# Optimization experiments

Measured on AMD Instinct MI355X. Metric: run time of the kernel, lower is better.

Reference implementation:

```python
import jax, jax.numpy as jnp
import numpy as np

B, N, HID, E, H = 4, 256, 256, 64, 4
OUT = HID // 2          # 128
D = OUT // H            # 32
AGG = H * (2 * D + 1)   # 260 = concat(mean D, attn_sum 1, max D) per head


def setup_inputs() -> dict:
    key = jax.random.key(0)
    ks = jax.random.split(key, 7)
    s = 0.05
    return {
        "h_x": jax.random.normal(ks[0], (B, N, HID), jnp.float32),
        "h_e": jax.random.normal(ks[1], (B, N, N, E), jnp.float32),
        "h_m": jnp.ones((B, N), jnp.float32),
        "W_Q": jax.random.normal(ks[2], (OUT, HID), jnp.float32) * s,
        "W_K": jax.random.normal(ks[3], (OUT, E), jnp.float32) * s,
        "W_V": jax.random.normal(ks[4], (OUT, E), jnp.float32) * s,
        "W_R": jax.random.normal(ks[5], (OUT, AGG), jnp.float32) * s,
    }


def reference(h_x, h_e, h_m, W_Q, W_K, W_V, W_R):
    # queries from node features: [B,H,N,D]
    h_q = (h_x @ W_Q.T).reshape(B, N, H, D).transpose(0, 2, 1, 3)
    # keys/values from dense pairwise edge features: [B,H,N,N,D]
    h_k = jnp.einsum('bnme,ce->bnmc', h_e, W_K).reshape(B, N, N, H, D).transpose(0, 3, 1, 2, 4)
    h_v = jnp.einsum('bnme,ce->bnmc', h_e, W_V).reshape(B, N, N, H, D).transpose(0, 3, 1, 2, 4)
    # broadcast dot: [B,H,N,N]
    scores = jnp.einsum('bhnd,bhnmd->bhnm', h_q, h_k) / np.float32(np.sqrt(D))
    # per-node mask broadcast as [B,1,N,1] (masks query rows)
    scores = jnp.where(h_m[:, None, :, None] == 0, -jnp.inf, scores)
    # NOTE: original code softmaxes over dim=1 = HEAD axis (faithful)
    attn = jax.nn.softmax(scores, axis=1)                      # [B,H,N,N]
    attn_w = attn[..., None] * h_v                             # [B,H,N,N,D]
    aggr_sum = attn_w.sum(axis=3)                              # [B,H,N,D]
    attn_sum = attn.sum(axis=3, keepdims=True) + 1e-8          # [B,H,N,1]
    aggr_mean = aggr_sum / attn_sum
    aggr_max = attn_w.max(axis=3)                              # [B,H,N,D]
    multi = jnp.concatenate([aggr_mean, attn_sum, aggr_max], axis=-1)  # [B,H,N,2D+1]
    aggr_out = multi.transpose(0, 2, 1, 3).reshape(B, N, AGG)  # [B,N,260]
    return aggr_out @ W_R.T                                    # [B,N,OUT]
```

## Files before the change

### kernel.cpp

```cpp
#include <hip/hip_runtime.h>
#include <hip/hip_bf16.h>

constexpr int Bb   = 4;
constexpr int Nn   = 256;
constexpr int HID  = 256;
constexpr int Ee   = 64;
constexpr int Hh   = 4;
constexpr int OUTc = 128;
constexpr int Dd   = 32;
constexpr int AGG  = 260;
constexpr int REC  = 264;
constexpr int QA_LD = 264;

constexpr size_t WS_WRT   = 0;
constexpr size_t WS_FRAGV = WS_WRT + (size_t)AGG * OUTc;
constexpr size_t WS_FRAGQ = WS_FRAGV + 4096;
constexpr size_t WS_UFRAG = WS_FRAGQ + 16384;

typedef __attribute__((ext_vector_type(8))) short short8;
typedef __attribute__((ext_vector_type(4))) float floatx4;

__device__ __forceinline__ unsigned pk2(float a, float b) {
    union { __hip_bfloat162 h; unsigned u; } cv;
    cv.h = __float22bfloat162_rn(float2{a, b});
    return cv.u;
}

__device__ __forceinline__ short8 pack8(floatx4 f0, floatx4 f1) {
    union { short8 s; unsigned u[4]; } r;
    r.u[0] = pk2(f0[0], f0[1]);
    r.u[1] = pk2(f0[2], f0[3]);
    r.u[2] = pk2(f1[0], f1[1]);
    r.u[3] = pk2(f1[2], f1[3]);
    return r.s;
}

__device__ __forceinline__ void gload16(const float* g, float* l) {
    __builtin_amdgcn_global_load_lds(
        (const __attribute__((address_space(1))) void*)g,
        (__attribute__((address_space(3))) void*)l, 16, 0, 0);
}

__global__ __launch_bounds__(256)
void eama_prep(const float* __restrict__ W_Q, const float* __restrict__ W_V,
               const float* __restrict__ W_R, const float* __restrict__ h_x,
               const float* __restrict__ W_K,
               unsigned short* __restrict__ wfragV, float* __restrict__ W_RT,
               unsigned short* __restrict__ ufrag)
{
    __shared__ __align__(16) unsigned short sA[16 * QA_LD];
    __shared__ __align__(16) float sqL[16][132];
    __shared__ __align__(16) float sU2[16][256];

    const int tid = threadIdx.x;
    const int bid = blockIdx.x;

    if (bid < 4) {
        const int e    = bid * 256 + tid;
        const int lane = e & 63;
        const int ks   = (e >> 6) & 1;
        const int ct   = e >> 7;
        const int ncol = lane & 15, q8 = lane >> 4;
        const float* row = W_V + (ct * 16 + ncol) * Ee;
        const int k0 = ks * 32 + q8 * 8;
        floatx4 f0 = *(const floatx4*)(row + k0);
        floatx4 f1 = *(const floatx4*)(row + k0 + 4);
        *(short8*)(wfragV + (size_t)e * 8) = pack8(f0, f1);
        return;
    }
    if (bid < 134) {
        const int i = (bid - 4) * 256 + tid;
        if (i < AGG * OUTc) {
            const int c = i & 127, j = i >> 7;
            W_RT[j * OUTc + c] = W_R[c * AGG + j];
        }
        return;
    }

    const int b0   = (bid - 134) * 16;
    const int lane = tid & 63;
    const int wv   = tid >> 6;
    const int ncol = lane & 15, q8 = lane >> 4;

    short8 bq[2][8];
    #pragma unroll
    for (int ct = 0; ct < 2; ++ct)
        #pragma unroll
        for (int ks = 0; ks < 8; ++ks) {
            const float* row = W_Q + (size_t)(wv * 32 + ct * 16 + ncol) * HID + ks * 32 + q8 * 8;
            bq[ct][ks] = pack8(*(const floatx4*)row, *(const floatx4*)(row + 4));
        }
    #pragma unroll
    for (int i = 0; i < 2; ++i) {
        const int idx = tid + i * 256;
        const int r = idx >> 5, blk = idx & 31;
        const float* src = h_x + (size_t)(b0 + r) * HID + blk * 8;
        floatx4 f0 = *(const floatx4*)(src);
        floatx4 f1 = *(const floatx4*)(src + 4);
        *(short8*)&sA[r * QA_LD + blk * 8] = pack8(f0, f1);
    }
    __syncthreads();
    floatx4 acc[2] = {(floatx4){0,0,0,0}, (floatx4){0,0,0,0}};
    #pragma unroll
    for (int ks = 0; ks < 8; ++ks) {
        short8 a = *(const short8*)&sA[ncol * QA_LD + ks * 32 + q8 * 8];
        acc[0] = __builtin_amdgcn_mfma_f32_16x16x32_bf16(a, bq[0][ks], acc[0], 0, 0, 0);
        acc[1] = __builtin_amdgcn_mfma_f32_16x16x32_bf16(a, bq[1][ks], acc[1], 0, 0, 0);
    }
    #pragma unroll
    for (int ct = 0; ct < 2; ++ct)
        #pragma unroll
        for (int rr = 0; rr < 4; ++rr)
            sqL[q8 * 4 + rr][wv * 32 + ct * 16 + ncol] = acc[ct][rr];
    __syncthreads();

    {
        const int h = wv, e = lane;
        float a16[16];
        #pragma unroll
        for (int i = 0; i < 16; ++i) a16[i] = 0.f;
        #pragma unroll
        for (int d4 = 0; d4 < 8; ++d4) {
            float wk0 = W_K[(h * Dd + d4 * 4 + 0) * Ee + e];
            float wk1 = W_K[(h * Dd + d4 * 4 + 1) * Ee + e];
            float wk2 = W_K[(h * Dd + d4 * 4 + 2) * Ee + e];
            float wk3 = W_K[(h * Dd + d4 * 4 + 3) * Ee + e];
            #pragma unroll
            for (int b16 = 0; b16 < 16; ++b16) {
                floatx4 qv = *(const floatx4*)&sqL[b16][h * Dd + d4 * 4];
                a16[b16] += (qv[0] * wk0 + qv[1] * wk1) + (qv[2] * wk2 + qv[3] * wk3);
            }
        }
        #pragma unroll
        for (int b16 = 0; b16 < 16; ++b16)
            sU2[b16][h * 64 + e] = a16[b16] * 0.1767766952966369f;
    }
    __syncthreads();

    #pragma unroll
    for (int k = 0; k < 8; ++k) {
        const int ei   = tid + k * 256;
        const int b16  = ei >> 7;
        const int rest = ei & 127;
        const int ks   = rest >> 6;
        const int l    = rest & 63;
        const int nc   = l & 15, qq = l >> 4;
        short8 v = {0, 0, 0, 0, 0, 0, 0, 0};
        if (nc < Hh) {
            floatx4 f0 = *(const floatx4*)&sU2[b16][nc * 64 + ks * 32 + qq * 8];
            floatx4 f1 = *(const floatx4*)&sU2[b16][nc * 64 + ks * 32 + qq * 8 + 4];
            v = pack8(f0, f1);
        }
        *(short8*)(ufrag + ((size_t)((b0 + b16) * 2 + ks) * 64 + l) * 8) = v;
    }
}

__global__ __launch_bounds__(256, 2)
void eama_full(const float* __restrict__ h_e, const float* __restrict__ h_m,
               const unsigned short* __restrict__ wfragV,
               const unsigned short* __restrict__ ufrag,
               const float* __restrict__ W_RT, float* __restrict__ out)
{
    __shared__ __align__(16) float sStage[4][2][4][64][4];
    __shared__ __align__(16) float sS[4][16][4];
    __shared__ float sVS[4][OUTc];
    __shared__ float sVM[4][OUTc];
    __shared__ float sAS[4][Hh];
    __shared__ float sAsum[Hh];

    float* sM = &sStage[0][0][0][0][0];
    float (*sAcc)[OUTc] = (float (*)[OUTc])(sM + 384);

    const int tid  = threadIdx.x;
    const int lane = tid & 63;
    const int w    = tid >> 6;
    const int ncol = lane & 15;
    const int q8   = lane >> 4;
    const int bn   = blockIdx.x;
    const float maskv = h_m[bn];

    short8 bfV[8][2];
    #pragma unroll
    for (int ct = 0; ct < 8; ++ct)
        #pragma unroll
        for (int ks = 0; ks < 2; ++ks)
            bfV[ct][ks] = *(const short8*)(wfragV + ((size_t)(ct * 2 + ks) * 64 + lane) * 8);
    short8 bu0 = *(const short8*)(ufrag + ((size_t)(bn * 2 + 0) * 64 + lane) * 8);
    short8 bu1 = *(const short8*)(ufrag + ((size_t)(bn * 2 + 1) * 64 + lane) * 8);
    asm volatile("" ::: "memory");

    const float* heb = h_e + (size_t)bn * Nn * Ee;
    const float* arq = heb + (size_t)(w * 64 + ncol) * Ee + q8 * 8;

    #define STAGE(it_, buf_) do { \
        const float* ar_ = arq + (size_t)(it_) * 16 * Ee; \
        gload16(ar_,      &sStage[w][buf_][0][0][0]); \
        gload16(ar_ + 4,  &sStage[w][buf_][1][0][0]); \
        gload16(ar_ + 32, &sStage[w][buf_][2][0][0]); \
        gload16(ar_ + 36, &sStage[w][buf_][3][0][0]); \
    } while (0)

    STAGE(0, 0);
    STAGE(1, 1);

    float vs[8], vm[8], asumH = 0.f;
    #pragma unroll
    for (int ct = 0; ct < 8; ++ct) { vs[ct] = 0.f; vm[ct] = -3.402823466e38f; }

    #pragma unroll
    for (int it = 0; it < 4; ++it) {
        const int buf = it & 1;
        if (it < 3) asm volatile("s_waitcnt vmcnt(4)" ::: "memory");
        else        asm volatile("s_waitcnt vmcnt(0)" ::: "memory");

        floatx4 c0 = *(const floatx4*)&sStage[w][buf][0][lane][0];
        floatx4 c1 = *(const floatx4*)&sStage[w][buf][1][lane][0];
        floatx4 c2 = *(const floatx4*)&sStage[w][buf][2][lane][0];
        floatx4 c3 = *(const floatx4*)&sStage[w][buf][3][lane][0];
        short8 af0 = pack8(c0, c1);
        short8 af1 = pack8(c2, c3);
        if (it < 2) {
            asm volatile("s_waitcnt lgkmcnt(0)" ::: "memory");
            STAGE(it + 2, buf);
        }

        floatx4 accV[8], accS = (floatx4){0, 0, 0, 0};
        #pragma unroll
        for (int ct = 0; ct < 8; ++ct) accV[ct] = (floatx4){0, 0, 0, 0};
        #pragma unroll
        for (int ct = 0; ct < 8; ++ct) {
            accV[ct] = __builtin_amdgcn_mfma_f32_16x16x32_bf16(af0, bfV[ct][0], accV[ct], 0, 0, 0);
            accV[ct] = __builtin_amdgcn_mfma_f32_16x16x32_bf16(af1, bfV[ct][1], accV[ct], 0, 0, 0);
        }
        accS = __builtin_amdgcn_mfma_f32_16x16x32_bf16(af0, bu0, accS, 0, 0, 0);
        accS = __builtin_amdgcn_mfma_f32_16x16x32_bf16(af1, bu1, accS, 0, 0, 0);

        if (ncol < Hh) {
            #pragma unroll
            for (int r = 0; r < 4; ++r)
                sS[w][q8 * 4 + r][ncol] = (maskv != 0.f) ? accS[r] : -1e30f;
        }
        __builtin_amdgcn_wave_barrier();

        #pragma unroll
        for (int r = 0; r < 4; ++r) {
            floatx4 sc = *(const floatx4*)&sS[w][q8 * 4 + r][0];
            float e0 = __expf(sc[0]), e1 = __expf(sc[1]);
            float e2 = __expf(sc[2]), e3 = __expf(sc[3]);
            float inv = 1.f / ((e0 + e1) + (e2 + e3));
            float a0 = e0 * inv, a1 = e1 * inv, a2 = e2 * inv, a3 = e3 * inv;
            asumH += (ncol & 2) ? ((ncol & 1) ? a3 : a2) : ((ncol & 1) ? a1 : a0);
            float p;
            p = a0 * accV[0][r]; vs[0] += p; vm[0] = fmaxf(vm[0], p);
            p = a0 * accV[1][r]; vs[1] += p; vm[1] = fmaxf(vm[1], p);
            p = a1 * accV[2][r]; vs[2] += p; vm[2] = fmaxf(vm[2], p);
            p = a1 * accV[3][r]; vs[3] += p; vm[3] = fmaxf(vm[3], p);
            p = a2 * accV[4][r]; vs[4] += p; vm[4] = fmaxf(vm[4], p);
            p = a2 * accV[5][r]; vs[5] += p; vm[5] = fmaxf(vm[5], p);
            p = a3 * accV[6][r]; vs[6] += p; vm[6] = fmaxf(vm[6], p);
            p = a3 * accV[7][r]; vs[7] += p; vm[7] = fmaxf(vm[7], p);
        }
        __builtin_amdgcn_wave_barrier();
    }
    #undef STAGE

    #pragma unroll
    for (int ct = 0; ct < 8; ++ct) {
        vs[ct] += __shfl_xor(vs[ct], 16, 64);
        vs[ct] += __shfl_xor(vs[ct], 32, 64);
        vm[ct] = fmaxf(vm[ct], __shfl_xor(vm[ct], 16, 64));
        vm[ct] = fmaxf(vm[ct], __shfl_xor(vm[ct], 32, 64));
    }
    asumH += __shfl_xor(asumH, 16, 64);
    asumH += __shfl_xor(asumH, 32, 64);

    if (lane < 16) {
        #pragma unroll
        for (int ct = 0; ct < 8; ++ct) {
            sVS[w][ct * 16 + lane] = vs[ct];
            sVM[w][ct * 16 + lane] = vm[ct];
        }
    }
    if (lane < Hh) sAS[w][lane] = asumH;
    __syncthreads();
    if (tid < Hh) {
        sAsum[tid] = 1e-8f +
            (sAS[0][tid] + sAS[1][tid]) + (sAS[2][tid] + sAS[3][tid]);
    }
    __syncthreads();
    if (tid < OUTc) {
        float vsum = (sVS[0][tid] + sVS[1][tid]) + (sVS[2][tid] + sVS[3][tid]);
        float vmax = fmaxf(fmaxf(sVM[0][tid], sVM[1][tid]), fmaxf(sVM[2][tid], sVM[3][tid]));
        const int h = tid >> 5, d = tid & 31;
        sM[h * 65 + d]      = vsum / sAsum[h];
        sM[h * 65 + 33 + d] = vmax;
        if (tid < Hh) sM[tid * 65 + 32] = sAsum[tid];
    }
    __syncthreads();
    {
        const int c = tid & 127, part = tid >> 7;
        const int j0 = part * 130;
        float a0 = 0.f, a1 = 0.f, a2 = 0.f, a3 = 0.f;
        #pragma unroll 4
        for (int j = j0; j < j0 + 128; j += 4) {
            a0 = fmaf(sM[j],     W_RT[(j)     * OUTc + c], a0);
            a1 = fmaf(sM[j + 1], W_RT[(j + 1) * OUTc + c], a1);
            a2 = fmaf(sM[j + 2], W_RT[(j + 2) * OUTc + c], a2);
            a3 = fmaf(sM[j + 3], W_RT[(j + 3) * OUTc + c], a3);
        }
        a0 = fmaf(sM[j0 + 128], W_RT[(j0 + 128) * OUTc + c], a0);
        a1 = fmaf(sM[j0 + 129], W_RT[(j0 + 129) * OUTc + c], a1);
        sAcc[part][c] = (a0 + a1) + (a2 + a3);
    }
    __syncthreads();
    if (tid < OUTc)
        out[bn * OUTc + tid] = sAcc[0][tid] + sAcc[1][tid];
}

extern "C" void kernel_launch(void* const* d_in, const int* in_sizes, int n_in,
                              void* d_out, int out_size, void* d_ws, size_t ws_size,
                              hipStream_t stream) {
    const float* h_x = (const float*)d_in[0];
    const float* h_e = (const float*)d_in[1];
    const float* h_m = (const float*)d_in[2];
    const float* W_Q = (const float*)d_in[3];
    const float* W_K = (const float*)d_in[4];
    const float* W_V = (const float*)d_in[5];
    const float* W_R = (const float*)d_in[6];
    float* out = (float*)d_out;

    float* ws            = (float*)d_ws;
    float* W_RT          = ws + WS_WRT;
    unsigned short* wfV  = (unsigned short*)(ws + WS_FRAGV);
    unsigned short* ufr  = (unsigned short*)(ws + WS_UFRAG);

    eama_prep<<<dim3(198), dim3(256), 0, stream>>>(W_Q, W_V, W_R, h_x, W_K, wfV, W_RT, ufr);
    eama_full<<<dim3(Bb * Nn), dim3(256), 0, stream>>>(h_e, h_m, wfV, ufr, W_RT, out);
}
```

Measured before the change: 127.4 us.

## Fuse prep kernel into main kernel, computing Q/U and V fragments per block

Removes the separate prep launch. Each block now builds its own W_V bf16 fragments through shared memory, computes its query row with W_Q and folds it with W_K into the score vector U. The output projection reads W_R directly with strided vector loads instead of a pre-transposed copy. This drops one launch, the workspace round trip and the dependency between the two kernels. In exchange every block redoes the weight packing and the small GEMVs, which adds redundant global loads and extra barriers before the main loop. Those prologue loads are issued after the first h_e stages, so they can overlap with them.

```diff
diff --git a/kernel.cpp b/kernel.cpp
--- a/kernel.cpp
+++ b/kernel.cpp
@@ -9,16 +9,10 @@
 constexpr int OUTc = 128;
 constexpr int Dd   = 32;
 constexpr int AGG  = 260;
-constexpr int REC  = 264;
-constexpr int QA_LD = 264;
-
-constexpr size_t WS_WRT   = 0;
-constexpr size_t WS_FRAGV = WS_WRT + (size_t)AGG * OUTc;
-constexpr size_t WS_FRAGQ = WS_FRAGV + 4096;
-constexpr size_t WS_UFRAG = WS_FRAGQ + 16384;
 
 typedef __attribute__((ext_vector_type(8))) short short8;
 typedef __attribute__((ext_vector_type(4))) float floatx4;
+typedef __attribute__((ext_vector_type(2))) float floatx2;
 
 __device__ __forceinline__ unsigned pk2(float a, float b) {
     union { __hip_bfloat162 h; unsigned u; } cv;
@@ -41,135 +35,17 @@
         (__attribute__((address_space(3))) void*)l, 16, 0, 0);
 }
 
-__global__ __launch_bounds__(256)
-void eama_prep(const float* __restrict__ W_Q, const float* __restrict__ W_V,
-               const float* __restrict__ W_R, const float* __restrict__ h_x,
-               const float* __restrict__ W_K,
-               unsigned short* __restrict__ wfragV, float* __restrict__ W_RT,
-               unsigned short* __restrict__ ufrag)
-{
-    __shared__ __align__(16) unsigned short sA[16 * QA_LD];
-    __shared__ __align__(16) float sqL[16][132];
-    __shared__ __align__(16) float sU2[16][256];
-
-    const int tid = threadIdx.x;
-    const int bid = blockIdx.x;
-
-    if (bid < 4) {
-        const int e    = bid * 256 + tid;
-        const int lane = e & 63;
-        const int ks   = (e >> 6) & 1;
-        const int ct   = e >> 7;
-        const int ncol = lane & 15, q8 = lane >> 4;
-        const float* row = W_V + (ct * 16 + ncol) * Ee;
-        const int k0 = ks * 32 + q8 * 8;
-        floatx4 f0 = *(const floatx4*)(row + k0);
-        floatx4 f1 = *(const floatx4*)(row + k0 + 4);
-        *(short8*)(wfragV + (size_t)e * 8) = pack8(f0, f1);
-        return;
-    }
-    if (bid < 134) {
-        const int i = (bid - 4) * 256 + tid;
-        if (i < AGG * OUTc) {
-            const int c = i & 127, j = i >> 7;
-            W_RT[j * OUTc + c] = W_R[c * AGG + j];
-        }
-        return;
-    }
-
-    const int b0   = (bid - 134) * 16;
-    const int lane = tid & 63;
-    const int wv   = tid >> 6;
-    const int ncol = lane & 15, q8 = lane >> 4;
-
-    short8 bq[2][8];
-    #pragma unroll
-    for (int ct = 0; ct < 2; ++ct)
-        #pragma unroll
-        for (int ks = 0; ks < 8; ++ks) {
-            const float* row = W_Q + (size_t)(wv * 32 + ct * 16 + ncol) * HID + ks * 32 + q8 * 8;
-            bq[ct][ks] = pack8(*(const floatx4*)row, *(const floatx4*)(row + 4));
-        }
-    #pragma unroll
-    for (int i = 0; i < 2; ++i) {
-        const int idx = tid + i * 256;
-        const int r = idx >> 5, blk = idx & 31;
-        const float* src = h_x + (size_t)(b0 + r) * HID + blk * 8;
-        floatx4 f0 = *(const floatx4*)(src);
-        floatx4 f1 = *(const floatx4*)(src + 4);
-        *(short8*)&sA[r * QA_LD + blk * 8] = pack8(f0, f1);
-    }
-    __syncthreads();
-    floatx4 acc[2] = {(floatx4){0,0,0,0}, (floatx4){0,0,0,0}};
-    #pragma unroll
-    for (int ks = 0; ks < 8; ++ks) {
-        short8 a = *(const short8*)&sA[ncol * QA_LD + ks * 32 + q8 * 8];
-        acc[0] = __builtin_amdgcn_mfma_f32_16x16x32_bf16(a, bq[0][ks], acc[0], 0, 0, 0);
-        acc[1] = __builtin_amdgcn_mfma_f32_16x16x32_bf16(a, bq[1][ks], acc[1], 0, 0, 0);
-    }
-    #pragma unroll
-    for (int ct = 0; ct < 2; ++ct)
-        #pragma unroll
-        for (int rr = 0; rr < 4; ++rr)
-            sqL[q8 * 4 + rr][wv * 32 + ct * 16 + ncol] = acc[ct][rr];
-    __syncthreads();
-
-    {
-        const int h = wv, e = lane;
-        float a16[16];
-        #pragma unroll
-        for (int i = 0; i < 16; ++i) a16[i] = 0.f;
-        #pragma unroll
-        for (int d4 = 0; d4 < 8; ++d4) {
-            float wk0 = W_K[(h * Dd + d4 * 4 + 0) * Ee + e];
-            float wk1 = W_K[(h * Dd + d4 * 4 + 1) * Ee + e];
-            float wk2 = W_K[(h * Dd + d4 * 4 + 2) * Ee + e];
-            float wk3 = W_K[(h * Dd + d4 * 4 + 3) * Ee + e];
-            #pragma unroll
-            for (int b16 = 0; b16 < 16; ++b16) {
-                floatx4 qv = *(const floatx4*)&sqL[b16][h * Dd + d4 * 4];
-                a16[b16] += (qv[0] * wk0 + qv[1] * wk1) + (qv[2] * wk2 + qv[3] * wk3);
-            }
-        }
-        #pragma unroll
-        for (int b16 = 0; b16 < 16; ++b16)
-            sU2[b16][h * 64 + e] = a16[b16] * 0.1767766952966369f;
-    }
-    __syncthreads();
-
-    #pragma unroll
-    for (int k = 0; k < 8; ++k) {
-        const int ei   = tid + k * 256;
-        const int b16  = ei >> 7;
-        const int rest = ei & 127;
-        const int ks   = rest >> 6;
-        const int l    = rest & 63;
-        const int nc   = l & 15, qq = l >> 4;
-        short8 v = {0, 0, 0, 0, 0, 0, 0, 0};
-        if (nc < Hh) {
-            floatx4 f0 = *(const floatx4*)&sU2[b16][nc * 64 + ks * 32 + qq * 8];
-            floatx4 f1 = *(const floatx4*)&sU2[b16][nc * 64 + ks * 32 + qq * 8 + 4];
-            v = pack8(f0, f1);
-        }
-        *(short8*)(ufrag + ((size_t)((b0 + b16) * 2 + ks) * 64 + l) * 8) = v;
-    }
-}
-
 __global__ __launch_bounds__(256, 2)
-void eama_full(const float* __restrict__ h_e, const float* __restrict__ h_m,
-               const unsigned short* __restrict__ wfragV,
-               const unsigned short* __restrict__ ufrag,
-               const float* __restrict__ W_RT, float* __restrict__ out)
+void eama_fused(const float* __restrict__ h_x, const float* __restrict__ h_e,
+                const float* __restrict__ h_m,
+                const float* __restrict__ W_Q, const float* __restrict__ W_K,
+                const float* __restrict__ W_V, const float* __restrict__ W_R,
+                float* __restrict__ out)
 {
     __shared__ __align__(16) float sStage[4][2][4][64][4];
     __shared__ __align__(16) float sS[4][16][4];
-    __shared__ float sVS[4][OUTc];
-    __shared__ float sVM[4][OUTc];
-    __shared__ float sAS[4][Hh];
-    __shared__ float sAsum[Hh];
-
-    float* sM = &sStage[0][0][0][0][0];
-    float (*sAcc)[OUTc] = (float (*)[OUTc])(sM + 384);
+    __shared__ __align__(16) unsigned short sWin[256 * 8];
+    __shared__ __align__(16) float sQp[256];
 
     const int tid  = threadIdx.x;
     const int lane = tid & 63;
@@ -179,16 +55,6 @@
     const int bn   = blockIdx.x;
     const float maskv = h_m[bn];
 
-    short8 bfV[8][2];
-    #pragma unroll
-    for (int ct = 0; ct < 8; ++ct)
-        #pragma unroll
-        for (int ks = 0; ks < 2; ++ks)
-            bfV[ct][ks] = *(const short8*)(wfragV + ((size_t)(ct * 2 + ks) * 64 + lane) * 8);
-    short8 bu0 = *(const short8*)(ufrag + ((size_t)(bn * 2 + 0) * 64 + lane) * 8);
-    short8 bu1 = *(const short8*)(ufrag + ((size_t)(bn * 2 + 1) * 64 + lane) * 8);
-    asm volatile("" ::: "memory");
-
     const float* heb = h_e + (size_t)bn * Nn * Ee;
     const float* arq = heb + (size_t)(w * 64 + ncol) * Ee + q8 * 8;
 
@@ -202,6 +68,64 @@
 
     STAGE(0, 0);
     STAGE(1, 1);
+
+    short8 bfV[8][2];
+    {
+        const int ncol_e = tid & 15;
+        const int q8_e   = (tid >> 4) & 3;
+        const int ks_e   = (tid >> 6) & 1;
+        const int cthi   = tid >> 7;
+        #pragma unroll
+        for (int c = 0; c < 4; ++c) {
+            const int ct = c * 2 + cthi;
+            const float* row = W_V + (size_t)(ct * 16 + ncol_e) * Ee + ks_e * 32 + q8_e * 8;
+            short8 v = pack8(*(const floatx4*)row, *(const floatx4*)(row + 4));
+            *(short8*)&sWin[tid * 8] = v;
+            __syncthreads();
+            #pragma unroll
+            for (int m = 0; m < 4; ++m)
+                bfV[c * 2 + (m >> 1)][m & 1] = *(const short8*)&sWin[(m * 64 + lane) * 8];
+            __syncthreads();
+        }
+    }
+
+    {
+        const int c = tid & 127, half = tid >> 7;
+        const float* wq = W_Q + (size_t)c * HID + half * 128;
+        const float* xr = h_x + (size_t)bn * HID + half * 128;
+        float acc = 0.f;
+        #pragma unroll
+        for (int i = 0; i < 32; ++i) {
+            floatx4 a = *(const floatx4*)(wq + i * 4);
+            floatx4 x = *(const floatx4*)(xr + i * 4);
+            acc = fmaf(a[0], x[0], fmaf(a[1], x[1], fmaf(a[2], x[2], fmaf(a[3], x[3], acc))));
+        }
+        sQp[tid] = acc;
+    }
+    __syncthreads();
+    if (tid < 128) sQp[tid] += sQp[tid + 128];
+    __syncthreads();
+
+    float* sU = &sS[0][0][0];
+    {
+        const int h = tid >> 6, e = tid & 63;
+        float acc = 0.f;
+        #pragma unroll
+        for (int d = 0; d < 32; ++d)
+            acc = fmaf(sQp[h * 32 + d], W_K[(size_t)(h * Dd + d) * Ee + e], acc);
+        sU[h * 64 + e] = acc * 0.1767766952966369f;
+    }
+    __syncthreads();
+
+    short8 bu0 = {0, 0, 0, 0, 0, 0, 0, 0};
+    short8 bu1 = {0, 0, 0, 0, 0, 0, 0, 0};
+    if (ncol < Hh) {
+        bu0 = pack8(*(const floatx4*)&sU[ncol * 64 + q8 * 8],
+                    *(const floatx4*)&sU[ncol * 64 + q8 * 8 + 4]);
+        bu1 = pack8(*(const floatx4*)&sU[ncol * 64 + 32 + q8 * 8],
+                    *(const floatx4*)&sU[ncol * 64 + 32 + q8 * 8 + 4]);
+    }
+    __syncthreads();
 
     float vs[8], vm[8], asumH = 0.f;
     #pragma unroll
@@ -274,47 +198,56 @@
     asumH += __shfl_xor(asumH, 16, 64);
     asumH += __shfl_xor(asumH, 32, 64);
 
+    float* SB = &sStage[0][0][0][0][0];
     if (lane < 16) {
         #pragma unroll
         for (int ct = 0; ct < 8; ++ct) {
-            sVS[w][ct * 16 + lane] = vs[ct];
-            sVM[w][ct * 16 + lane] = vm[ct];
-        }
-    }
-    if (lane < Hh) sAS[w][lane] = asumH;
+            SB[w * 2048 + ct * 16 + lane]       = vs[ct];
+            SB[w * 2048 + 128 + ct * 16 + lane] = vm[ct];
+        }
+    }
+    if (lane < Hh) SB[w * 2048 + 256 + lane] = asumH;
     __syncthreads();
     if (tid < Hh) {
-        sAsum[tid] = 1e-8f +
-            (sAS[0][tid] + sAS[1][tid]) + (sAS[2][tid] + sAS[3][tid]);
+        SB[512 + tid] = 1e-8f +
+            (SB[0 * 2048 + 256 + tid] + SB[1 * 2048 + 256 + tid]) +
+            (SB[2 * 2048 + 256 + tid] + SB[3 * 2048 + 256 + tid]);
     }
     __syncthreads();
     if (tid < OUTc) {
-        float vsum = (sVS[0][tid] + sVS[1][tid]) + (sVS[2][tid] + sVS[3][tid]);
-        float vmax = fmaxf(fmaxf(sVM[0][tid], sVM[1][tid]), fmaxf(sVM[2][tid], sVM[3][tid]));
+        float vsum = (SB[0 * 2048 + tid] + SB[1 * 2048 + tid]) +
+                     (SB[2 * 2048 + tid] + SB[3 * 2048 + tid]);
+        float vmax = fmaxf(fmaxf(SB[0 * 2048 + 128 + tid], SB[1 * 2048 + 128 + tid]),
+                           fmaxf(SB[2 * 2048 + 128 + tid], SB[3 * 2048 + 128 + tid]));
         const int h = tid >> 5, d = tid & 31;
-        sM[h * 65 + d]      = vsum / sAsum[h];
-        sM[h * 65 + 33 + d] = vmax;
-        if (tid < Hh) sM[tid * 65 + 32] = sAsum[tid];
+        SB[768 + h * 65 + d]      = vsum / SB[512 + h];
+        SB[768 + h * 65 + 33 + d] = vmax;
+        if (tid < Hh) SB[768 + tid * 65 + 32] = SB[512 + tid];
     }
     __syncthreads();
     {
         const int c = tid & 127, part = tid >> 7;
         const int j0 = part * 130;
+        const float* wr = W_R + (size_t)c * AGG + j0;
+        const float* sM = SB + 768;
         float a0 = 0.f, a1 = 0.f, a2 = 0.f, a3 = 0.f;
-        #pragma unroll 4
-        for (int j = j0; j < j0 + 128; j += 4) {
-            a0 = fmaf(sM[j],     W_RT[(j)     * OUTc + c], a0);
-            a1 = fmaf(sM[j + 1], W_RT[(j + 1) * OUTc + c], a1);
-            a2 = fmaf(sM[j + 2], W_RT[(j + 2) * OUTc + c], a2);
-            a3 = fmaf(sM[j + 3], W_RT[(j + 3) * OUTc + c], a3);
-        }
-        a0 = fmaf(sM[j0 + 128], W_RT[(j0 + 128) * OUTc + c], a0);
-        a1 = fmaf(sM[j0 + 129], W_RT[(j0 + 129) * OUTc + c], a1);
-        sAcc[part][c] = (a0 + a1) + (a2 + a3);
+        #pragma unroll 8
+        for (int j = 0; j < 128; j += 4) {
+            floatx2 A  = *(const floatx2*)(wr + j);
+            floatx2 Bv = *(const floatx2*)(wr + j + 2);
+            a0 = fmaf(sM[j0 + j],     A[0],  a0);
+            a1 = fmaf(sM[j0 + j + 1], A[1],  a1);
+            a2 = fmaf(sM[j0 + j + 2], Bv[0], a2);
+            a3 = fmaf(sM[j0 + j + 3], Bv[1], a3);
+        }
+        floatx2 T = *(const floatx2*)(wr + 128);
+        a0 = fmaf(sM[j0 + 128], T[0], a0);
+        a1 = fmaf(sM[j0 + 129], T[1], a1);
+        SB[1100 + part * 128 + c] = (a0 + a1) + (a2 + a3);
     }
     __syncthreads();
     if (tid < OUTc)
-        out[bn * OUTc + tid] = sAcc[0][tid] + sAcc[1][tid];
+        out[(size_t)bn * OUTc + tid] = SB[1100 + tid] + SB[1100 + 128 + tid];
 }
 
 extern "C" void kernel_launch(void* const* d_in, const int* in_sizes, int n_in,
@@ -329,11 +262,6 @@
     const float* W_R = (const float*)d_in[6];
     float* out = (float*)d_out;
 
-    float* ws            = (float*)d_ws;
-    float* W_RT          = ws + WS_WRT;
-    unsigned short* wfV  = (unsigned short*)(ws + WS_FRAGV);
-    unsigned short* ufr  = (unsigned short*)(ws + WS_UFRAG);
-
-    eama_prep<<<dim3(198), dim3(256), 0, stream>>>(W_Q, W_V, W_R, h_x, W_K, wfV, W_RT, ufr);
-    eama_full<<<dim3(Bb * Nn), dim3(256), 0, stream>>>(h_e, h_m, wfV, ufr, W_RT, out);
-}
+    eama_fused<<<dim3(Bb * Nn), dim3(256), 0, stream>>>(
+        h_x, h_e, h_m, W_Q, W_K, W_V, W_R, out);
+}
```

Result: slower. 141.2 us (+10.8%).
